# Kernel optimization log

Measured on AMD Instinct MI355X. Metric: run time of the kernel, lower is better.

The kernel has to match this reference:

```python
import jax, jax.numpy as jnp
import numpy as np

N = 50000
E = 600000
D_IN = 128
D_HID = 128
D_OUT = 128


def _glorot(key, shape):
    fan_in, fan_out = shape[0], shape[1]
    lim = float(np.sqrt(6.0 / (fan_in + fan_out)))
    return jax.random.uniform(key, shape, jnp.float32, -lim, lim)


def setup_inputs() -> dict:
    key = jax.random.key(0)
    ks = jax.random.split(key, 10)
    x = jax.random.normal(ks[0], (N, D_IN), jnp.float32)
    edge_index = jax.random.randint(ks[1], (2, E), 0, N, jnp.int64)
    # layer 1 params
    W_pool1 = _glorot(ks[2], (D_IN, D_HID))
    b_pool1 = jnp.zeros((D_HID,), jnp.float32)
    W_upd1 = _glorot(ks[3], (D_IN + D_HID, D_HID))
    b_upd1 = jnp.zeros((D_HID,), jnp.float32)
    # layer 2 params
    W_pool2 = _glorot(ks[4], (D_HID, D_OUT))
    b_pool2 = jnp.zeros((D_OUT,), jnp.float32)
    W_upd2 = _glorot(ks[5], (D_HID + D_OUT, D_OUT))
    b_upd2 = jnp.zeros((D_OUT,), jnp.float32)
    return {
        "x": x, "edge_index": edge_index,
        "W_pool1": W_pool1, "b_pool1": b_pool1, "W_upd1": W_upd1, "b_upd1": b_upd1,
        "W_pool2": W_pool2, "b_pool2": b_pool2, "W_upd2": W_upd2, "b_upd2": b_upd2,
    }


def _pool_sage_conv(x, src, dst, W_pool, b_pool, W_upd, b_upd):
    # message: ReLU(W_pool x_j + b) on gathered source features  [E, out]
    msg = jax.nn.relu(x[src] @ W_pool + b_pool)
    # aggregate: element-wise max over incoming edges per destination node
    agg = jax.ops.segment_max(msg, dst, num_segments=x.shape[0])
    # nodes with no in-edges get -inf from segment_max; torch code zeros non-finite
    agg = jnp.where(jnp.isfinite(agg), agg, jnp.zeros_like(agg))
    # update: ReLU(W_upd [x_v ; h_N(v)] + b)
    out = jax.nn.relu(jnp.concatenate([x, agg], axis=-1) @ W_upd + b_upd)
    return out


def reference(x, edge_index,
              W_pool1, b_pool1, W_upd1, b_upd1,
              W_pool2, b_pool2, W_upd2, b_upd2):
    src, dst = edge_index[0], edge_index[1]
    h = _pool_sage_conv(x, src, dst, W_pool1, b_pool1, W_upd1, b_upd1)
    h = _pool_sage_conv(h, src, dst, W_pool2, b_pool2, W_upd2, b_upd2)
    return h
```

## Files before the change

### kernel.cpp

```cpp
#include <hip/hip_runtime.h>

#define D 128
#define SLOTS 64
#define SLOTP 66
#define NBUCK 800
#define BSLOT 1024
#define EPB 8192

typedef __attribute__((ext_vector_type(8))) short bf16x8;
typedef __attribute__((ext_vector_type(4))) float f32x4;
typedef __attribute__((ext_vector_type(8))) unsigned short u16x8;

__device__ __forceinline__ unsigned short f2bf(float f) {
    unsigned u = __float_as_uint(f);
    u = u + 0x7fffu + ((u >> 16) & 1u);
    return (unsigned short)(u >> 16);
}

__device__ __forceinline__ void pack_one(const float* __restrict__ W,
                                         unsigned short* __restrict__ out, int g, int l) {
    const int kt = g >> 3, nt = g & 7;
    u16x8 pv;
#pragma unroll
    for (int j = 0; j < 8; ++j)
        pv[j] = f2bf(W[(size_t)(kt * 32 + (l >> 4) * 8 + j) * D + nt * 16 + (l & 15)]);
    *(u16x8*)&out[((size_t)g * 64 + l) * 8] = pv;
}

__global__ void prep_kernel(const float4* __restrict__ x4, ushort4* __restrict__ xb4, int n4,
                            const float* __restrict__ Wp1, const float* __restrict__ Wu1,
                            const float* __restrict__ Wp2, const float* __restrict__ Wu2,
                            unsigned short* __restrict__ Wp1p, unsigned short* __restrict__ Wu1p,
                            unsigned short* __restrict__ Wp2p, unsigned short* __restrict__ Wu2p,
                            const int* __restrict__ src, const int* __restrict__ dst,
                            int* __restrict__ gcur, int* __restrict__ bebuf, int E,
                            int EB1, int CB) {
    int b = blockIdx.x;
    const int t = threadIdx.x;
    if (b < EB1) {
        __shared__ int hist[NBUCK];
        __shared__ int boff[NBUCK];
        for (int i = t; i < NBUCK; i += 256) hist[i] = 0;
        __syncthreads();
        const int4* dst4 = (const int4*)dst;
        const int4* src4 = (const int4*)src;
        const int q0 = b * (EPB / 4);
        const int nq = (E + 3) / 4;
#pragma unroll
        for (int k = 0; k < EPB / 4; k += 256) {
            int qi = q0 + k + t;
            if (qi < nq) {
                int4 d4 = dst4[qi];
                int e = qi * 4;
                if (e + 0 < E) atomicAdd(&hist[d4.x >> 6], 1);
                if (e + 1 < E) atomicAdd(&hist[d4.y >> 6], 1);
                if (e + 2 < E) atomicAdd(&hist[d4.z >> 6], 1);
                if (e + 3 < E) atomicAdd(&hist[d4.w >> 6], 1);
            }
        }
        __syncthreads();
        {
            const int off = (b * 311) % NBUCK;
            for (int k = t; k < NBUCK; k += 256) {
                int i = k + off;
                if (i >= NBUCK) i -= NBUCK;
                int c = hist[i];
                boff[i] = c ? atomicAdd(&gcur[i], c) : 0;
                hist[i] = 0;
            }
        }
        __syncthreads();
#pragma unroll
        for (int k = 0; k < EPB / 4; k += 256) {
            int qi = q0 + k + t;
            if (qi < nq) {
                int4 d4 = dst4[qi];
                int4 s4 = src4[qi];
                int e = qi * 4;
#pragma unroll
                for (int j = 0; j < 4; ++j) {
                    int dd = (j == 0) ? d4.x : (j == 1) ? d4.y : (j == 2) ? d4.z : d4.w;
                    int ss = (j == 0) ? s4.x : (j == 1) ? s4.y : (j == 2) ? s4.z : s4.w;
                    if (e + j < E) {
                        int bk = dd >> 6;
                        int r = atomicAdd(&hist[bk], 1);
                        int pos = boff[bk] + r;
                        if (pos < BSLOT)
                            bebuf[(size_t)bk * BSLOT + pos] = (ss & 0xFFFF) | ((dd & 63) << 16);
                    }
                }
            }
        }
        return;
    }
    b -= EB1;
    if (b < CB) {
        int i = b * 256 + t;
        if (i < n4) {
            float4 v = x4[i];
            ushort4 o;
            o.x = f2bf(v.x); o.y = f2bf(v.y); o.z = f2bf(v.z); o.w = f2bf(v.w);
            xb4[i] = o;
        }
        return;
    }
    b -= CB;
    {
        int g = b * 4 + (t >> 6);
        int l = t & 63;
        if (g < 32)       pack_one(Wp1, Wp1p, g, l);
        else if (g < 96)  pack_one(Wu1, Wu1p, g - 32, l);
        else if (g < 128) pack_one(Wp2, Wp2p, g - 96, l);
        else if (g < 192) pack_one(Wu2, Wu2p, g - 128, l);
    }
}

__launch_bounds__(256)
__global__ void pool_mfma(const unsigned short* __restrict__ X0,
                          const unsigned short* __restrict__ Wp,
                          const float* __restrict__ bias,
                          unsigned short* __restrict__ OUT, int n) {
    __shared__ unsigned short tlds[4][16 * D];
    const int t = threadIdx.x, w = t >> 6, l = t & 63;
    const int lrow = l & 15, lk = l >> 4;
    const int r0 = blockIdx.x * 64 + w * 16;
    int arow = r0 + lrow;
    if (arow > n - 1) arow = n - 1;

    f32x4 acc[8];
#pragma unroll
    for (int nt = 0; nt < 8; ++nt) {
        float bv = bias[nt * 16 + lrow];
        acc[nt] = (f32x4){bv, bv, bv, bv};
    }
#pragma unroll
    for (int kt = 0; kt < 4; ++kt) {
        bf16x8 a = *(const bf16x8*)(X0 + (size_t)arow * D + kt * 32 + lk * 8);
#pragma unroll
        for (int nt = 0; nt < 8; ++nt) {
            bf16x8 b = *(const bf16x8*)(Wp + (((size_t)kt * 8 + nt) * 64 + l) * 8);
            acc[nt] = __builtin_amdgcn_mfma_f32_16x16x32_bf16(a, b, acc[nt], 0, 0, 0);
        }
    }
    unsigned short* tt = tlds[w];
#pragma unroll
    for (int nt = 0; nt < 8; ++nt)
#pragma unroll
        for (int r = 0; r < 4; ++r)
            tt[(lk * 4 + r) * D + nt * 16 + lrow] = f2bf(fmaxf(acc[nt][r], 0.f));
    __syncthreads();
#pragma unroll
    for (int p = 0; p < 4; ++p) {
        int flat = p * 512 + l * 8;
        int rt = flat >> 7, col = flat & (D - 1);
        int grow = r0 + rt;
        if (grow < n)
            *(u16x8*)(OUT + (size_t)grow * D + col) = *(const u16x8*)(tt + flat);
    }
}


__device__ __forceinline__ void build_lists512(const int* __restrict__ gcur,
                                               const int* __restrict__ bebuf,
                                               int* h2_s, unsigned short* slots_s,
                                               int bid, int t) {
    if (t < 64) h2_s[t] = 0;
    __syncthreads();
    int cnt = gcur[bid];
    if (cnt > BSLOT) cnt = BSLOT;
    const int* bb = bebuf + (size_t)bid * BSLOT;
    for (int i = t; i < cnt; i += 512) {
        int pk = bb[i];
        int nl = pk >> 16;
        int r = atomicAdd(&h2_s[nl], 1);
        if (r < SLOTS) slots_s[nl * SLOTP + r] = (unsigned short)(pk & 0xFFFF);
    }
    __syncthreads();
}

__device__ __forceinline__ void agg512(const int* h2_s, const unsigned short* slots_s,
                                       const u16x8* __restrict__ P8,
                                       unsigned short* A_s, int t) {
    const int nl = t >> 3;
    const int q = t & 7;
    u16x8 m0[2], m1[2];
#pragma unroll
    for (int c = 0; c < 2; ++c) { m0[c] = (u16x8){0,0,0,0,0,0,0,0}; m1[c] = m0[c]; }
    int d = h2_s[nl];
    if (d > SLOTS) d = SLOTS;
    const unsigned short* sp = slots_s + nl * SLOTP;
    int j = 0;
    for (; j + 1 < d; j += 2) {
        const u16x8* pa = P8 + (size_t)sp[j] * 16 + q * 2;
        const u16x8* pb = P8 + (size_t)sp[j + 1] * 16 + q * 2;
        u16x8 a0 = pa[0], a1 = pa[1];
        u16x8 b0 = pb[0], b1 = pb[1];
        m0[0] = __builtin_elementwise_max(m0[0], a0);
        m0[1] = __builtin_elementwise_max(m0[1], a1);
        m1[0] = __builtin_elementwise_max(m1[0], b0);
        m1[1] = __builtin_elementwise_max(m1[1], b1);
    }
    if (j < d) {
        const u16x8* pa = P8 + (size_t)sp[j] * 16 + q * 2;
        m0[0] = __builtin_elementwise_max(m0[0], pa[0]);
        m0[1] = __builtin_elementwise_max(m0[1], pa[1]);
    }
    m0[0] = __builtin_elementwise_max(m0[0], m1[0]);
    m0[1] = __builtin_elementwise_max(m0[1], m1[1]);
#pragma unroll
    for (int c = 0; c < 2; ++c) {
        int col = q * 16 + c * 8;
        *(u16x8*)&A_s[nl * D + (col ^ ((nl & 7) << 3))] = m0[c];
    }
}

__device__ __forceinline__ bf16x8 lds_afrag(const unsigned short* S, int row, int kbase) {
    return *(const bf16x8*)&S[row * D + (kbase ^ ((row & 7) << 3))];
}

__launch_bounds__(512)
__global__ void fused_upd_pool(const unsigned short* __restrict__ xb,
                               const u16x8* __restrict__ Pb8,
                               const unsigned short* __restrict__ Wu1p, const float* __restrict__ bu1,
                               const unsigned short* __restrict__ Wp2p, const float* __restrict__ bp2,
                               const int* __restrict__ gcur, const int* __restrict__ bebuf,
                               unsigned short* __restrict__ Hb, unsigned short* __restrict__ P2b,
                               int n) {
    __shared__ unsigned short A_s[64 * D];
    __shared__ unsigned short H_s[64 * D];
    unsigned short* slots_s = H_s;
    int* h2_s = (int*)(H_s + 64 * SLOTP);
    const int t = threadIdx.x, w = t >> 6, l = t & 63;
    const int base = blockIdx.x * 64;
    const int lrow = l & 15, lk = l >> 4;
    const int s = w & 3, h = w >> 2;

    const int r0 = base + s * 16;
    int arow = r0 + lrow;
    if (arow > n - 1) arow = n - 1;

    bf16x8 a_pre[4];
#pragma unroll
    for (int kt = 0; kt < 4; ++kt)
        a_pre[kt] = *(const bf16x8*)(xb + (size_t)arow * D + kt * 32 + lk * 8);

    build_lists512(gcur, bebuf, h2_s, slots_s, blockIdx.x, t);
    agg512(h2_s, slots_s, Pb8, A_s, t);
    __syncthreads();

    f32x4 acc[4];
#pragma unroll
    for (int ntl = 0; ntl < 4; ++ntl) {
        float bv = bu1[(h * 4 + ntl) * 16 + lrow];
        acc[ntl] = (f32x4){bv, bv, bv, bv};
    }
#pragma unroll
    for (int kt = 0; kt < 4; ++kt) {
#pragma unroll
        for (int ntl = 0; ntl < 4; ++ntl) {
            bf16x8 b = *(const bf16x8*)(Wu1p + (((size_t)kt * 8 + h * 4 + ntl) * 64 + l) * 8);
            acc[ntl] = __builtin_amdgcn_mfma_f32_16x16x32_bf16(a_pre[kt], b, acc[ntl], 0, 0, 0);
        }
    }
#pragma unroll
    for (int kt = 4; kt < 8; ++kt) {
        bf16x8 a = lds_afrag(A_s, s * 16 + lrow, (kt - 4) * 32 + lk * 8);
#pragma unroll
        for (int ntl = 0; ntl < 4; ++ntl) {
            bf16x8 b = *(const bf16x8*)(Wu1p + (((size_t)kt * 8 + h * 4 + ntl) * 64 + l) * 8);
            acc[ntl] = __builtin_amdgcn_mfma_f32_16x16x32_bf16(a, b, acc[ntl], 0, 0, 0);
        }
    }

#pragma unroll
    for (int ntl = 0; ntl < 4; ++ntl)
#pragma unroll
        for (int r = 0; r < 4; ++r) {
            int row = s * 16 + lk * 4 + r;
            int col = (h * 4 + ntl) * 16 + lrow;
            H_s[row * D + (col ^ ((row & 7) << 3))] = f2bf(fmaxf(acc[ntl][r], 0.f));
        }
    __syncthreads();

#pragma unroll
    for (int p = 0; p < 2; ++p) {
        int flat = p * 4096 + t * 8;
        int rt = flat >> 7, col = flat & (D - 1);
        int grow = base + rt;
        if (grow < n)
            *(u16x8*)(Hb + (size_t)grow * D + col) =
                *(const u16x8*)&H_s[rt * D + (col ^ ((rt & 7) << 3))];
    }

    f32x4 acc2[4];
#pragma unroll
    for (int ntl = 0; ntl < 4; ++ntl) {
        float bv = bp2[(h * 4 + ntl) * 16 + lrow];
        acc2[ntl] = (f32x4){bv, bv, bv, bv};
    }
#pragma unroll
    for (int kt = 0; kt < 4; ++kt) {
        bf16x8 a = lds_afrag(H_s, s * 16 + lrow, kt * 32 + lk * 8);
#pragma unroll
        for (int ntl = 0; ntl < 4; ++ntl) {
            bf16x8 b = *(const bf16x8*)(Wp2p + (((size_t)kt * 8 + h * 4 + ntl) * 64 + l) * 8);
            acc2[ntl] = __builtin_amdgcn_mfma_f32_16x16x32_bf16(a, b, acc2[ntl], 0, 0, 0);
        }
    }
#pragma unroll
    for (int ntl = 0; ntl < 4; ++ntl)
#pragma unroll
        for (int r = 0; r < 4; ++r) {
            int row = s * 16 + lk * 4 + r;
            int col = (h * 4 + ntl) * 16 + lrow;
            A_s[row * D + (col ^ ((row & 7) << 3))] = f2bf(fmaxf(acc2[ntl][r], 0.f));
        }
    __syncthreads();
#pragma unroll
    for (int p = 0; p < 2; ++p) {
        int flat = p * 4096 + t * 8;
        int rt = flat >> 7, col = flat & (D - 1);
        int grow = base + rt;
        if (grow < n)
            *(u16x8*)(P2b + (size_t)grow * D + col) =
                *(const u16x8*)&A_s[rt * D + (col ^ ((rt & 7) << 3))];
    }
}

__launch_bounds__(512)
__global__ void fused_upd2(const unsigned short* __restrict__ Hb,
                           const u16x8* __restrict__ P2b8,
                           const unsigned short* __restrict__ Wu2p, const float* __restrict__ bu2,
                           const int* __restrict__ gcur, const int* __restrict__ bebuf,
                           float* __restrict__ out, int n) {
    __shared__ __align__(16) unsigned char smem[64 * D * 4];
    unsigned short* A_s = (unsigned short*)smem;
    unsigned short* slots_s = (unsigned short*)(smem + 64 * D * 2);
    int* h2_s = (int*)(smem + 64 * D * 2 + 64 * SLOTP * 2);
    float* T_s = (float*)smem;
    const int t = threadIdx.x, w = t >> 6, l = t & 63;
    const int base = blockIdx.x * 64;
    const int lrow = l & 15, lk = l >> 4;
    const int s = w & 3, h = w >> 2;

    const int r0 = base + s * 16;
    int arow = r0 + lrow;
    if (arow > n - 1) arow = n - 1;

    bf16x8 a_pre[4];
#pragma unroll
    for (int kt = 0; kt < 4; ++kt)
        a_pre[kt] = *(const bf16x8*)(Hb + (size_t)arow * D + kt * 32 + lk * 8);

    build_lists512(gcur, bebuf, h2_s, slots_s, blockIdx.x, t);
    agg512(h2_s, slots_s, P2b8, A_s, t);
    __syncthreads();

    f32x4 acc[4];
#pragma unroll
    for (int ntl = 0; ntl < 4; ++ntl) {
        float bv = bu2[(h * 4 + ntl) * 16 + lrow];
        acc[ntl] = (f32x4){bv, bv, bv, bv};
    }
#pragma unroll
    for (int kt = 0; kt < 4; ++kt) {
#pragma unroll
        for (int ntl = 0; ntl < 4; ++ntl) {
            bf16x8 b = *(const bf16x8*)(Wu2p + (((size_t)kt * 8 + h * 4 + ntl) * 64 + l) * 8);
            acc[ntl] = __builtin_amdgcn_mfma_f32_16x16x32_bf16(a_pre[kt], b, acc[ntl], 0, 0, 0);
        }
    }
#pragma unroll
    for (int kt = 4; kt < 8; ++kt) {
        bf16x8 a = lds_afrag(A_s, s * 16 + lrow, (kt - 4) * 32 + lk * 8);
#pragma unroll
        for (int ntl = 0; ntl < 4; ++ntl) {
            bf16x8 b = *(const bf16x8*)(Wu2p + (((size_t)kt * 8 + h * 4 + ntl) * 64 + l) * 8);
            acc[ntl] = __builtin_amdgcn_mfma_f32_16x16x32_bf16(a, b, acc[ntl], 0, 0, 0);
        }
    }
    __syncthreads();

#pragma unroll
    for (int ntl = 0; ntl < 4; ++ntl)
#pragma unroll
        for (int r = 0; r < 4; ++r) {
            int row = s * 16 + lk * 4 + r;
            int col = (h * 4 + ntl) * 16 + lrow;
            T_s[row * D + col] = fmaxf(acc[ntl][r], 0.f);
        }
    __syncthreads();
#pragma unroll
    for (int p = 0; p < 4; ++p) {
        int flat = p * 2048 + t * 4;
        int rt = flat >> 7, col = flat & (D - 1);
        int grow = base + rt;
        if (grow < n)
            *(float4*)(out + (size_t)grow * D + col) = *(const float4*)(T_s + flat);
    }
}

extern "C" void kernel_launch(void* const* d_in, const int* in_sizes, int n_in,
                              void* d_out, int out_size, void* d_ws, size_t ws_size,
                              hipStream_t stream) {
    const float* x   = (const float*)d_in[0];
    const int*   ei  = (const int*)d_in[1];
    const float* Wp1 = (const float*)d_in[2];
    const float* bp1 = (const float*)d_in[3];
    const float* Wu1 = (const float*)d_in[4];
    const float* bu1 = (const float*)d_in[5];
    const float* Wp2 = (const float*)d_in[6];
    const float* bp2 = (const float*)d_in[7];
    const float* Wu2 = (const float*)d_in[8];
    const float* bu2 = (const float*)d_in[9];
    float* out = (float*)d_out;

    const int n = in_sizes[0] / D;
    const int E = in_sizes[1] / 2;
    const int* src = ei;
    const int* dst = ei + E;

    unsigned short* xb   = (unsigned short*)d_ws;
    unsigned short* Pb   = xb + (size_t)n * D;
    unsigned short* Hb   = Pb + (size_t)n * D;
    unsigned short* P2b  = Hb + (size_t)n * D;
    unsigned short* Wp1p = P2b + (size_t)n * D;
    unsigned short* Wu1p = Wp1p + D * D;
    unsigned short* Wp2p = Wu1p + 2 * D * D;
    unsigned short* Wu2p = Wp2p + D * D;
    int* gcur  = (int*)(Wu2p + 2 * D * D);
    int* bebuf = gcur + NBUCK;

    const int gb  = (n + 63) / 64;
    const int CB  = (n * D / 4 + 255) / 256;
    const int PB  = 48;
    const int EB1 = (E + EPB - 1) / EPB;

    hipMemsetAsync(gcur, 0, NBUCK * sizeof(int), stream);
    prep_kernel<<<EB1 + CB + PB, 256, 0, stream>>>(
        (const float4*)x, (ushort4*)xb, n * D / 4,
        Wp1, Wu1, Wp2, Wu2, Wp1p, Wu1p, Wp2p, Wu2p, src, dst, gcur, bebuf, E, EB1, CB);

    pool_mfma<<<gb, 256, 0, stream>>>(xb, Wp1p, bp1, Pb, n);
    fused_upd_pool<<<gb, 512, 0, stream>>>(xb, (const u16x8*)Pb, Wu1p, bu1, Wp2p, bp2,
                                           gcur, bebuf, Hb, P2b, n);
    fused_upd2<<<gb, 512, 0, stream>>>(Hb, (const u16x8*)P2b, Wu2p, bu2,
                                       gcur, bebuf, out, n);
}
```

Baseline: 114.5 us.

## Move edge binning into pool kernel and fold memset into prep launch

Edge bucketing now runs as extra blocks inside the first pool GEMM kernel instead of inside the prep kernel. The gcur memset becomes one block of the prep kernel. Edges per binning block drop from 8192 to 4096, which doubles the number of binning blocks. This removes a memset launch, lets the binning overlap with the layer-1 pool MFMA work, and shortens the prep kernel. The cost is more shared memory per pool block (hist/boff added to tlds), which may lower occupancy, and more global atomics on gcur.

Result: faster. 102.5 us (median of 2 runs) (-10.5%).

```diff
diff --git a/kernel.cpp b/kernel.cpp
--- a/kernel.cpp
+++ b/kernel.cpp
@@ -5,7 +5,7 @@
 #define SLOTP 66
 #define NBUCK 800
 #define BSLOT 1024
-#define EPB 8192
+#define EPB 4096
 
 typedef __attribute__((ext_vector_type(8))) short bf16x8;
 typedef __attribute__((ext_vector_type(4))) float f32x4;
@@ -27,19 +27,50 @@
     *(u16x8*)&out[((size_t)g * 64 + l) * 8] = pv;
 }
 
-__global__ void prep_kernel(const float4* __restrict__ x4, ushort4* __restrict__ xb4, int n4,
-                            const float* __restrict__ Wp1, const float* __restrict__ Wu1,
-                            const float* __restrict__ Wp2, const float* __restrict__ Wu2,
-                            unsigned short* __restrict__ Wp1p, unsigned short* __restrict__ Wu1p,
-                            unsigned short* __restrict__ Wp2p, unsigned short* __restrict__ Wu2p,
-                            const int* __restrict__ src, const int* __restrict__ dst,
-                            int* __restrict__ gcur, int* __restrict__ bebuf, int E,
-                            int EB1, int CB) {
+__global__ void prep2_kernel(const float4* __restrict__ x4, ushort4* __restrict__ xb4, int n4,
+                             const float* __restrict__ Wp1, const float* __restrict__ Wu1,
+                             const float* __restrict__ Wp2, const float* __restrict__ Wu2,
+                             unsigned short* __restrict__ Wp1p, unsigned short* __restrict__ Wu1p,
+                             unsigned short* __restrict__ Wp2p, unsigned short* __restrict__ Wu2p,
+                             int* __restrict__ gcur, int CB, int PB) {
     int b = blockIdx.x;
     const int t = threadIdx.x;
-    if (b < EB1) {
-        __shared__ int hist[NBUCK];
-        __shared__ int boff[NBUCK];
+    if (b < CB) {
+        int i = b * 256 + t;
+        if (i < n4) {
+            float4 v = x4[i];
+            ushort4 o;
+            o.x = f2bf(v.x); o.y = f2bf(v.y); o.z = f2bf(v.z); o.w = f2bf(v.w);
+            xb4[i] = o;
+        }
+        return;
+    }
+    b -= CB;
+    if (b < PB) {
+        int g = b * 4 + (t >> 6);
+        int l = t & 63;
+        if (g < 32)       pack_one(Wp1, Wp1p, g, l);
+        else if (g < 96)  pack_one(Wu1, Wu1p, g - 32, l);
+        else if (g < 128) pack_one(Wp2, Wp2p, g - 96, l);
+        else if (g < 192) pack_one(Wu2, Wu2p, g - 128, l);
+        return;
+    }
+    for (int i = t; i < NBUCK; i += 256) gcur[i] = 0;
+}
+
+__launch_bounds__(256)
+__global__ void poolbin_kernel(const unsigned short* __restrict__ X0,
+                               const unsigned short* __restrict__ Wp,
+                               const float* __restrict__ bias,
+                               unsigned short* __restrict__ OUT, int n,
+                               const int* __restrict__ src, const int* __restrict__ dst,
+                               int* __restrict__ gcur, int* __restrict__ bebuf, int E, int EB1) {
+    __shared__ int hist[NBUCK];
+    __shared__ int boff[NBUCK];
+    __shared__ unsigned short tlds[4][16 * D];
+    const int t = threadIdx.x;
+    if (blockIdx.x < EB1) {
+        const int b = blockIdx.x;
         for (int i = t; i < NBUCK; i += 256) hist[i] = 0;
         __syncthreads();
         const int4* dst4 = (const int4*)dst;
@@ -93,37 +124,10 @@
         }
         return;
     }
-    b -= EB1;
-    if (b < CB) {
-        int i = b * 256 + t;
-        if (i < n4) {
-            float4 v = x4[i];
-            ushort4 o;
-            o.x = f2bf(v.x); o.y = f2bf(v.y); o.z = f2bf(v.z); o.w = f2bf(v.w);
-            xb4[i] = o;
-        }
-        return;
-    }
-    b -= CB;
-    {
-        int g = b * 4 + (t >> 6);
-        int l = t & 63;
-        if (g < 32)       pack_one(Wp1, Wp1p, g, l);
-        else if (g < 96)  pack_one(Wu1, Wu1p, g - 32, l);
-        else if (g < 128) pack_one(Wp2, Wp2p, g - 96, l);
-        else if (g < 192) pack_one(Wu2, Wu2p, g - 128, l);
-    }
-}
-
-__launch_bounds__(256)
-__global__ void pool_mfma(const unsigned short* __restrict__ X0,
-                          const unsigned short* __restrict__ Wp,
-                          const float* __restrict__ bias,
-                          unsigned short* __restrict__ OUT, int n) {
-    __shared__ unsigned short tlds[4][16 * D];
-    const int t = threadIdx.x, w = t >> 6, l = t & 63;
+    const int bid = blockIdx.x - EB1;
+    const int w = t >> 6, l = t & 63;
     const int lrow = l & 15, lk = l >> 4;
-    const int r0 = blockIdx.x * 64 + w * 16;
+    const int r0 = bid * 64 + w * 16;
     int arow = r0 + lrow;
     if (arow > n - 1) arow = n - 1;
 
@@ -436,12 +440,13 @@
     const int PB  = 48;
     const int EB1 = (E + EPB - 1) / EPB;
 
-    hipMemsetAsync(gcur, 0, NBUCK * sizeof(int), stream);
-    prep_kernel<<<EB1 + CB + PB, 256, 0, stream>>>(
+    prep2_kernel<<<CB + PB + 1, 256, 0, stream>>>(
         (const float4*)x, (ushort4*)xb, n * D / 4,
-        Wp1, Wu1, Wp2, Wu2, Wp1p, Wu1p, Wp2p, Wu2p, src, dst, gcur, bebuf, E, EB1, CB);
-
-    pool_mfma<<<gb, 256, 0, stream>>>(xb, Wp1p, bp1, Pb, n);
+        Wp1, Wu1, Wp2, Wu2, Wp1p, Wu1p, Wp2p, Wu2p, gcur, CB, PB);
+
+    poolbin_kernel<<<EB1 + gb, 256, 0, stream>>>(
+        xb, Wp1p, bp1, Pb, n, src, dst, gcur, bebuf, E, EB1);
+
     fused_upd_pool<<<gb, 512, 0, stream>>>(xb, (const u16x8*)Pb, Wu1p, bu1, Wp2p, bp2,
                                            gcur, bebuf, Hb, P2b, n);
     fused_upd2<<<gb, 512, 0, stream>>>(Hb, (const u16x8*)P2b, Wu2p, bu2,
```
